# Kernel tuning notes

Measured on AMD Instinct MI355X. Metric: run time of the kernel, lower is better.

## Reference

```python
import jax, jax.numpy as jnp
import numpy as np

K = 2  # diffusion order
N, S, D, L, C = 4000, 32, 128, 2, 10
THETA = 0.5


def setup_inputs() -> dict:
    key = jax.random.key(0)
    ks = jax.random.split(key, 16)
    w = 0.05  # weight scale to keep tanh/exp in sane range
    return {
        "A": jax.random.uniform(ks[0], (N, N), dtype=jnp.float32),
        "embs": jax.random.normal(ks[1], (L, S, N, D), dtype=jnp.float32),
        "conv1_w": jax.random.normal(ks[2], (K, D, D), dtype=jnp.float32) * w,
        "conv2_w": jax.random.normal(ks[3], (K, D, D), dtype=jnp.float32) * w,
        "lin_in_w": jax.random.normal(ks[4], (D, D), dtype=jnp.float32) * w,
        "lin_out_w": jax.random.normal(ks[5], (D, 2 * D), dtype=jnp.float32) * w,
        "W_psi": jax.random.normal(ks[6], (2 * D, D), dtype=jnp.float32) * w,
        "b_psi": jax.random.normal(ks[7], (D,), dtype=jnp.float32) * w,
        "ae": jax.random.uniform(ks[8], (N, 1, 1), dtype=jnp.float32),
        "ab": jax.random.uniform(ks[9], (N, 1, 1), dtype=jnp.float32),
        "emb_table": jax.random.uniform(ks[10], (N, D), minval=-0.1, maxval=0.1, dtype=jnp.float32),
        "W_p": jax.random.normal(ks[11], (D, C), dtype=jnp.float32) * w,
        "W_c": jax.random.normal(ks[12], (D, D), dtype=jnp.float32) * w,
    }


def _diffusion(A_tilde, X, W):
    # A_tilde: [N,N] (sym-normalized); X: [N,S,D] (linear in X, so batching over S
    # is identical to the per-timestep loop); W: [K,D,D]
    P_f = A_tilde / A_tilde.sum(axis=1, keepdims=True)
    P_v = A_tilde.T / A_tilde.sum(axis=0, keepdims=True)
    Z = jnp.einsum('mn,nsd->msd', P_f, X) @ W[0]
    P_psi_f, P_psi_v = P_f, P_v
    for k in range(1, K):
        if k < K // 2:
            P_psi_f = P_psi_f @ P_f
            M = P_psi_f
        else:
            P_psi_v = P_psi_v @ P_v
            M = P_psi_v
        Z = Z + jnp.einsum('mn,nsd->msd', M, X) @ W[k]
    return Z


def _attention(context, lin_in_w, lin_out_w, ae, ab):
    # context: [N,S,D]; query is the last timestep, output_len == 1
    q = context[:, -1, :] @ lin_in_w.T                    # [N,D]
    scores = jnp.einsum('nd,nsd->ns', q, context)         # [N,S]
    attw = jax.nn.softmax(scores, axis=-1)                # [N,S]
    mix = attw[:, None, :] * context.transpose(0, 2, 1)   # [N,D,S]
    delta_t = jnp.arange(S - 1, -1, -1, dtype=context.dtype)  # flipped arange
    bt = jnp.exp(-ab * delta_t[None, None, :])            # [N,1,S]
    term2 = jax.nn.relu(ae * mix * bt)                    # [N,D,S]
    mix_sum = (term2 + mix).sum(axis=-1)                  # [N,D]
    combined = jnp.concatenate([mix_sum, q], axis=-1)     # [N,2D]
    return jnp.tanh(combined @ lin_out_w.T)               # [N,D]


def reference(A, embs, conv1_w, conv2_w, lin_in_w, lin_out_w, W_psi, b_psi,
              ae, ab, emb_table, W_p, W_c):
    n = A.shape[0]
    A_t = A + jnp.eye(n, dtype=A.dtype)
    d_inv_sqrt = A_t.sum(axis=1) ** -0.5
    A_tilde = d_inv_sqrt[:, None] * A_t * d_inv_sqrt[None, :]

    outs = []
    for l in range(L):
        X = embs[l].transpose(1, 0, 2)                    # [N,S,D]
        h = _diffusion(A_tilde, X, conv1_w)
        h = jax.nn.relu(h)
        h = _diffusion(A_tilde, h, conv2_w)               # [N,S,D]
        # fusion with theta = 0.5 (h_tilde is the raw embedding)
        fused = jnp.concatenate([THETA * h, (1.0 - THETA) * X], axis=-1) @ W_psi + b_psi
        outs.append(_attention(fused, lin_in_w, lin_out_w, ae, ab))
    outputs = jnp.stack(outs)                             # [L,N,D]

    # embedding lookup over arange(N) is an identity gather
    qs = jax.nn.relu(emb_table)                           # [N,D]
    betas = jnp.exp(jnp.einsum('nd,lne->lde', qs, jnp.tanh(outputs)))  # [L,D,D]
    betas = betas / betas.sum(axis=0)
    Z = jnp.einsum('lnd,lde->ne', outputs, betas)         # [N,D]

    P = jax.nn.softmax(Z @ W_p, axis=1)                   # [N,C]
    C_mat = P.T @ Z                                       # [C,D]
    eta = P.T @ A @ P                                     # [C,C] (vectorized eta_ij)
    C_prime = jax.nn.relu(eta @ (C_mat @ W_c.T))          # [C,D]
    return P @ C_prime                                    # [N,D]
```

## Files before the change

### kernel.cpp

```cpp
#include <hip/hip_runtime.h>
#include <hip/hip_bf16.h>


typedef __attribute__((ext_vector_type(8))) short short8;
typedef __attribute__((ext_vector_type(4))) float f32x4;
typedef __attribute__((ext_vector_type(4))) unsigned short us4;

__device__ __forceinline__ unsigned short f2bf(float x) {
  unsigned int u = __builtin_bit_cast(unsigned int, x);
  u += 0x7FFFu + ((u >> 16) & 1u);
  return (unsigned short)(u >> 16);
}
__device__ __forceinline__ float bf2f(unsigned short u) {
  unsigned int x = ((unsigned int)u) << 16;
  return __builtin_bit_cast(float, x);
}

__device__ __forceinline__ void gload16(const void* g, void* l) {
  __builtin_amdgcn_global_load_lds((const __attribute__((address_space(1))) void*)g,
                                   (__attribute__((address_space(3))) void*)l, 16, 0, 0);
}

__device__ __forceinline__ void barrier_() {
  __builtin_amdgcn_sched_barrier(0);
  asm volatile("" ::: "memory");
  __builtin_amdgcn_s_barrier();
  asm volatile("" ::: "memory");
  __builtin_amdgcn_sched_barrier(0);
}

template<int TRANS, int RELU>
__global__ __launch_bounds__(512, 2)
void gemm256(const unsigned short* __restrict__ Ap, int lda,
             const unsigned short* __restrict__ Bp, int ldb,
             unsigned short* __restrict__ outp, int ldo, int K)
{
  __shared__ alignas(16) unsigned short lds[81920];
  const int t = threadIdx.x;
  const int lane = t & 63;
  const int wave = t >> 6;
  const int wm = wave >> 2;
  const int wn = wave & 3;
  const int lrow = lane & 15;
  const int kgrp = lane >> 4;
  const int slotbase = (kgrp ^ (lrow & 7)) << 3;

  const int b = blockIdx.x;
  const int wg = (b & 7) * 32 + (b >> 3);
  const int m0 = (wg >> 4) << 8;
  const int j0 = (wg & 15) << 8;

  const int prow = t >> 3;
  const int lslot = (t & 7) ^ (prow & 7);
  const unsigned short* srcA = Ap + (size_t)(m0 + prow) * lda + lslot * 8;
  const unsigned short* srcB = Bp + (size_t)(j0 + prow) * ldb + lslot * 8;
  const size_t a64 = (size_t)64 * lda, a128 = (size_t)128 * lda;
  const size_t b64 = (size_t)64 * ldb, b128 = (size_t)128 * ldb;
  unsigned short* dA = &lds[t * 8];
  unsigned short* dB = &lds[32768 + t * 8];
  const int NT = K >> 6;

#define STG_A(h, kb, kt) { const unsigned short* s_ = srcA + (h)*a128 + (size_t)(kt)*64; \
    gload16(s_, dA + (kb)*16384 + (h)*8192); \
    gload16(s_ + a64, dA + (kb)*16384 + (h)*8192 + 4096); }
#define STG_B(h, bb, kt) { const unsigned short* s_ = srcB + (h)*b128 + (size_t)(kt)*64; \
    gload16(s_, dB + (bb)*16384 + (h)*8192); \
    gload16(s_ + b64, dB + (bb)*16384 + (h)*8192 + 4096); }

  const int arb = wm * 8192 + lrow * 64 + slotbase;
  const int brb = (wn >> 1) * 8192 + ((wn & 1) << 12) + lrow * 64 + slotbase;

#define RD_A(dst, base_off) \
  _Pragma("unroll") for (int mf_ = 0; mf_ < 4; ++mf_) { \
    dst[mf_][0] = *(const short8*)&lds[(base_off) + mf_*1024]; \
    dst[mf_][1] = *(const short8*)&lds[((base_off) ^ 32) + mf_*1024]; }
#define RD_B(dst, base_off) \
  _Pragma("unroll") for (int nf_ = 0; nf_ < 2; ++nf_) { \
    dst[nf_][0] = *(const short8*)&lds[(base_off) + nf_*1024]; \
    dst[nf_][1] = *(const short8*)&lds[((base_off) ^ 32) + nf_*1024]; }

#define MFMA16(AF, BF, MB, NB) \
  _Pragma("unroll") for (int mf_ = 0; mf_ < 4; ++mf_) \
  _Pragma("unroll") for (int nf_ = 0; nf_ < 2; ++nf_) { \
    acc[(MB)+mf_][(NB)+nf_] = __builtin_amdgcn_mfma_f32_16x16x32_bf16(AF[mf_][0], BF[nf_][0], acc[(MB)+mf_][(NB)+nf_], 0,0,0); \
    acc[(MB)+mf_][(NB)+nf_] = __builtin_amdgcn_mfma_f32_16x16x32_bf16(AF[mf_][1], BF[nf_][1], acc[(MB)+mf_][(NB)+nf_], 0,0,0); }

#define LGKM(n) { asm volatile("s_waitcnt lgkmcnt(" #n ")" ::: "memory"); \
                  __builtin_amdgcn_sched_barrier(0); }

  f32x4 acc[8][4];
#pragma unroll
  for (int i = 0; i < 8; ++i)
#pragma unroll
    for (int j = 0; j < 4; ++j) acc[i][j] = f32x4{0.f, 0.f, 0.f, 0.f};

  short8 a0[4][2], a1[4][2], b0[2][2], b1[2][2];

  STG_B(0, 0, 0); STG_B(1, 0, 0); STG_A(0, 0, 0); STG_A(1, 0, 0);
  STG_B(0, 1, 1); STG_B(1, 1, 1); STG_A(0, 1, 1); STG_A(1, 1, 1);
  asm volatile("s_waitcnt vmcnt(8)" ::: "memory");
  barrier_();
  RD_A(a0, arb);
  RD_B(b0, 32768 + brb);

  int rb3 = 0, rn3 = 1, sb3 = 2;
  for (int V = 0; V < NT; ++V) {
    const int abuf  = (V & 1) << 14;
    const int anbuf = ((V + 1) & 1) << 14;
    const int bbuf  = 32768 + (rb3 << 14);
    const int bnbuf = 32768 + (rn3 << 14);
    const bool stg = (V + 2 < NT);
    const bool rdn = (V + 1 < NT);

    RD_B(b1, bbuf + brb + 2048);
    LGKM(4);
    if (stg) STG_B(0, sb3, V + 2);
    __builtin_amdgcn_s_setprio(1);
    MFMA16(a0, b0, 0, 0);
    __builtin_amdgcn_s_setprio(0);
    barrier_();

    RD_A(a1, abuf + arb + 4096);
    LGKM(8);
    if (stg) STG_B(1, sb3, V + 2);
    __builtin_amdgcn_s_setprio(1);
    MFMA16(a0, b1, 0, 2);
    __builtin_amdgcn_s_setprio(0);
    if (stg) { asm volatile("s_waitcnt vmcnt(4)" ::: "memory"); }
    else     { asm volatile("s_waitcnt vmcnt(0)" ::: "memory"); }
    barrier_();

    if (rdn) { RD_A(a0, anbuf + arb); LGKM(8); }
    else     { LGKM(0); }
    if (stg) STG_A(0, (V & 1), V + 2);
    __builtin_amdgcn_s_setprio(1);
    MFMA16(a1, b0, 4, 0);
    __builtin_amdgcn_s_setprio(0);
    barrier_();

    if (rdn) { RD_B(b0, bnbuf + brb); LGKM(4); }
    else     { LGKM(0); }
    if (stg) STG_A(1, (V & 1), V + 2);
    __builtin_amdgcn_s_setprio(1);
    MFMA16(a1, b1, 4, 2);
    __builtin_amdgcn_s_setprio(0);
    barrier_();

    rb3 = rn3; rn3 = (rn3 == 2) ? 0 : rn3 + 1;
    sb3 = (sb3 == 2) ? 0 : sb3 + 1;
  }

#pragma unroll
  for (int mf = 0; mf < 8; ++mf) {
#pragma unroll
    for (int nf = 0; nf < 4; ++nf) {
      const int m = m0 + wm * 128 + mf * 16 + kgrp * 4;
      const int j = j0 + wn * 64 + nf * 16 + lrow;
      if (TRANS) {
        us4 pk;
#pragma unroll
        for (int r = 0; r < 4; ++r) pk[r] = f2bf(acc[mf][nf][r]);
        *(us4*)(outp + (size_t)j * ldo + m) = pk;
      } else {
#pragma unroll
        for (int r = 0; r < 4; ++r) {
          float v = acc[mf][nf][r];
          if (RELU) v = fmaxf(v, 0.f);
          outp[(size_t)(m + r) * ldo + j] = f2bf(v);
        }
      }
    }
  }
#undef STG_A
#undef STG_B
#undef RD_A
#undef RD_B
#undef MFMA16
#undef LGKM
}

template<int EPI, int KFULL, int MINB>
__global__ __launch_bounds__(256, MINB)
void gemm_smallk(const unsigned short* __restrict__ A1,
                 const unsigned short* __restrict__ A2,
                 int k_switch, int a_zstride, int lda,
                 const unsigned short* __restrict__ B, int ldb,
                 void* __restrict__ outp,
                 long o_j, long o_m, long o_z, long o_jt,
                 const float* __restrict__ bias)
{
  __shared__ alignas(16) unsigned short At[(KFULL / 32) * 4096];
  __shared__ alignas(16) unsigned short Bt[(KFULL / 32) * 4096];
  const int t = threadIdx.x;
  const int lane = t & 63;
  const int wave = t >> 6;
  const int m0 = blockIdx.x << 7;
  const int jt = blockIdx.y;
  const int j0 = jt << 7;
  const int z  = blockIdx.z;
  const int wm = (wave >> 1) << 6;
  const int wn = (wave & 1) << 6;
  const int lrow = lane & 15;
  const int kgrp = lane >> 4;

  const unsigned short* A1z = A1 + (long)z * a_zstride;
  const unsigned short* A2z = A2 + (long)z * a_zstride;

  const int r0 = t >> 2, q0 = t & 3;
  const int c1 = t + 256;
  const int r1 = c1 >> 2, q1 = c1 & 3;

#pragma unroll
  for (int kk = 0; kk < KFULL / 32; ++kk) {
    const int k0 = kk * 32;
    const unsigned short* As; int ka;
    if (k0 < k_switch) { As = A1z; ka = k0; } else { As = A2z; ka = k0 - k_switch; }
    gload16(As + (long)(m0 + r0) * lda + ka + q0 * 8, At + kk * 4096 + t * 8);
    gload16(As + (long)(m0 + r1) * lda + ka + q1 * 8, At + kk * 4096 + c1 * 8);
    gload16(B  + (long)(j0 + r0) * ldb + k0 + q0 * 8, Bt + kk * 4096 + t * 8);
    gload16(B  + (long)(j0 + r1) * ldb + k0 + q1 * 8, Bt + kk * 4096 + c1 * 8);
  }
  __syncthreads();

  f32x4 acc[4][4];
#pragma unroll
  for (int i = 0; i < 4; ++i)
#pragma unroll
    for (int j = 0; j < 4; ++j) acc[i][j] = f32x4{0.f, 0.f, 0.f, 0.f};

#pragma unroll
  for (int kk = 0; kk < KFULL / 32; ++kk) {
    short8 af[4], bv[4];
#pragma unroll
    for (int i = 0; i < 4; ++i)
      af[i] = *(const short8*)(At + kk * 4096 + (wm + i * 16 + lrow) * 32 + kgrp * 8);
#pragma unroll
    for (int i = 0; i < 4; ++i)
      bv[i] = *(const short8*)(Bt + kk * 4096 + (wn + i * 16 + lrow) * 32 + kgrp * 8);
#pragma unroll
    for (int i = 0; i < 4; ++i)
#pragma unroll
      for (int j = 0; j < 4; ++j)
        acc[i][j] = __builtin_amdgcn_mfma_f32_16x16x32_bf16(af[i], bv[j], acc[i][j], 0, 0, 0);
  }

  const int mlb = wm + kgrp * 4;
#pragma unroll
  for (int i = 0; i < 4; ++i) {
#pragma unroll
    for (int j = 0; j < 4; ++j) {
      const int jl = wn + j * 16 + lrow;
      const int ml = mlb + i * 16;
      if (EPI == 0) {
        long base = (long)jl * o_j + (long)(m0 + ml) * o_m + (long)z * o_z + (long)jt * o_jt;
        us4 pk;
#pragma unroll
        for (int r = 0; r < 4; ++r) pk[r] = f2bf(acc[i][j][r]);
        *(us4*)((unsigned short*)outp + base) = pk;
      } else if (EPI == 2) {
        float* of = (float*)outp;
        float badd = bias[j0 + jl];
#pragma unroll
        for (int r = 0; r < 4; ++r) {
          long idx = (long)jl * o_j + (long)(m0 + ml + r) * o_m + (long)z * o_z + (long)jt * o_jt;
          of[idx] = acc[i][j][r] + badd;
        }
      } else {
        float* of = (float*)outp;
#pragma unroll
        for (int r = 0; r < 4; ++r) {
          int mm = m0 + ml + r;
          int n = mm & 4095, l = mm >> 12;
          if (n < 4000)
            of[(size_t)l * 512000 + (size_t)n * 128 + (j0 + jl)] = tanhf(acc[i][j][r]);
        }
      }
    }
  }
}

__global__ __launch_bounds__(256) void rowsum_dis(const float* __restrict__ A,
                                                  float* __restrict__ dis) {
  int m = blockIdx.x;
  if (m >= 4000) { if (threadIdx.x == 0) dis[m] = 0.f; return; }
  const float* r = A + (long)m * 4000;
  float a = 0.f;
  for (int i = threadIdx.x; i < 1000; i += 256) {
    float4 v = ((const float4*)r)[i];
    a += v.x + v.y + v.z + v.w;
  }
  for (int o = 32; o; o >>= 1) a += __shfl_xor(a, o);
  __shared__ float ls[4];
  if ((threadIdx.x & 63) == 0) ls[threadIdx.x >> 6] = a;
  __syncthreads();
  if (threadIdx.x == 0) dis[m] = rsqrtf(1.f + ls[0] + ls[1] + ls[2] + ls[3]);
}

__global__ __launch_bounds__(256) void wrow_kernel(const float* __restrict__ A,
                                                   const float* __restrict__ dis,
                                                   float* __restrict__ iwrow) {
  int m = blockIdx.x;
  if (m >= 4000) { if (threadIdx.x == 0) iwrow[m] = 0.f; return; }
  const float* r = A + (long)m * 4000;
  float a = 0.f;
  for (int n = threadIdx.x; n < 4000; n += 256) a += r[n] * dis[n];
  for (int o = 32; o; o >>= 1) a += __shfl_xor(a, o);
  __shared__ float ls[4];
  if ((threadIdx.x & 63) == 0) ls[threadIdx.x >> 6] = a;
  __syncthreads();
  if (threadIdx.x == 0) iwrow[m] = 1.f / (ls[0] + ls[1] + ls[2] + ls[3] + dis[m]);
}

__global__ __launch_bounds__(256) void wcol_part(const float* __restrict__ A,
                                                 const float* __restrict__ dis,
                                                 float* __restrict__ part) {
  int j = blockIdx.x * 256 + threadIdx.x;
  int mz = blockIdx.y;
  float a = 0.f;
  if (j < 4000) {
    int ms = mz * 125;
    for (int m = ms; m < ms + 125; ++m) a += A[(long)m * 4000 + j] * dis[m];
  }
  part[(long)mz * 4096 + j] = a;
}

__global__ __launch_bounds__(256) void wcol_fin(const float* __restrict__ part,
                                                const float* __restrict__ dis,
                                                float* __restrict__ iwcol) {
  int j = blockIdx.x * 256 + threadIdx.x;
  float s = 0.f;
  for (int z = 0; z < 32; ++z) s += part[(long)z * 4096 + j];
  iwcol[j] = (j < 4000) ? 1.f / (s + dis[j]) : 0.f;
}

__global__ __launch_bounds__(256) void build_P(const float* __restrict__ A,
                                               const float* __restrict__ dis,
                                               const float* __restrict__ iwrow,
                                               const float* __restrict__ iwcol,
                                               unsigned short* __restrict__ Pcat,
                                               unsigned short* __restrict__ PV,
                                               unsigned short* __restrict__ PVT) {
  __shared__ float tile[64][65];
  int m0 = blockIdx.y * 64, n0 = blockIdx.x * 64;
#pragma unroll
  for (int i = 0; i < 16; ++i) {
    int idx = i * 256 + threadIdx.x;
    int lr = idx >> 6, lc = idx & 63;
    int m = m0 + lr, n = n0 + lc;
    float v = 0.f;
    if (m < 4000 && n < 4000) {
      float a = A[(long)m * 4000 + n];
      if (m == n) a += 1.f;
      v = a * dis[n];
    }
    Pcat[(long)m * 8192 + n] = f2bf(v * iwrow[m]);
    float pv = v * iwcol[m];
    PVT[(long)m * 4096 + n] = f2bf(pv);
    tile[lr][lc] = pv;
  }
  __syncthreads();
#pragma unroll
  for (int i = 0; i < 16; ++i) {
    int idx = i * 256 + threadIdx.x;
    int lr = idx >> 6, lc = idx & 63;
    PV[(long)(n0 + lr) * 4096 + (m0 + lc)] = f2bf(tile[lc][lr]);
  }
}

__global__ __launch_bounds__(256) void prep_weights(const float* __restrict__ lin_out,
                                                    const float* __restrict__ c1,
                                                    const float* __restrict__ c2,
                                                    const float* __restrict__ wpsi,
                                                    unsigned short* __restrict__ CW1T,
                                                    unsigned short* __restrict__ CW2T,
                                                    unsigned short* __restrict__ WPST,
                                                    unsigned short* __restrict__ LWOB) {
  int i = blockIdx.x * 256 + threadIdx.x;
  if (i < 32768) {
    int j = i >> 7, kk = i & 127;
    CW1T[i] = f2bf(c1[(j >> 7) * 16384 + kk * 128 + (j & 127)]);
  } else if (i < 65536) {
    int k = i - 32768; int j = k >> 7, kk = k & 127;
    CW2T[k] = f2bf(c2[(j >> 7) * 16384 + kk * 128 + (j & 127)]);
  } else if (i < 98304) {
    int k = i - 65536; int e = k >> 8, d2 = k & 255;
    WPST[k] = f2bf(0.5f * wpsi[d2 * 128 + e]);
  } else if (i < 131072) {
    int k = i - 98304;
    LWOB[k] = f2bf(lin_out[k]);
  }
}

__global__ __launch_bounds__(256) void wq_prep(const float* __restrict__ lin_in,
                                               const float* __restrict__ bpsi,
                                               const unsigned short* __restrict__ WPST,
                                               unsigned short* __restrict__ WQ,
                                               float* __restrict__ BQ) {
  int b = blockIdx.x, t = threadIdx.x;
  if (b < 128) {
    int idx = b * 256 + t;
    int d = idx >> 8, k2 = idx & 255;
    float acc = 0.f;
    for (int e = 0; e < 128; ++e)
      acc += lin_in[d * 128 + e] * bf2f(WPST[e * 256 + k2]);
    WQ[idx] = f2bf(acc);
  } else if (t < 128) {
    float acc = 0.f;
    for (int e = 0; e < 128; ++e) acc += bpsi[e] * lin_in[t * 128 + e];
    BQ[t] = acc;
  }
}

__global__ __launch_bounds__(256) void convert_X(const float* __restrict__ embsL,
                                                 unsigned short* __restrict__ X) {
  long i4 = (long)blockIdx.x * 256 + threadIdx.x;
  long e = i4 << 2;
  int n = (int)(e >> 12);
  int r = (int)(e & 4095);
  us4 o;
  if (n < 4000) {
    int s = r >> 7, d = r & 127;
    float4 v = *(const float4*)(embsL + ((long)s * 4000 + n) * 128 + d);
    o[0] = f2bf(v.x); o[1] = f2bf(v.y); o[2] = f2bf(v.z); o[3] = f2bf(v.w);
  } else { o[0] = o[1] = o[2] = o[3] = 0; }
  *(us4*)(X + (long)n * 4096 + r) = o;
}

__global__ __launch_bounds__(128) void attention2(const float* __restrict__ F,
                                                  const float* __restrict__ Q,
                                                  const float* __restrict__ ae,
                                                  const float* __restrict__ ab,
                                                  unsigned short* __restrict__ CATl) {
  int n = blockIdx.x, t = threadIdx.x;
  if (n >= 4000) {
    CATl[(size_t)n * 256 + t] = 0;
    CATl[(size_t)n * 256 + 128 + t] = 0;
    return;
  }
  __shared__ float Fs[32 * 132];
  __shared__ float qv[128], attw[32], btv[32];
  const float* Fr = F + (long)n * 4096;
  for (int i = t; i < 4096; i += 128) { int s = i >> 7, d = i & 127; Fs[s * 132 + d] = Fr[i]; }
  qv[t] = Q[(long)n * 128 + t];
  __syncthreads();
  if (t < 32) {
    float sc = 0.f;
    for (int d = 0; d < 128; ++d) sc += qv[d] * Fs[t * 132 + d];
    float mx = sc;
    for (int o = 16; o; o >>= 1) mx = fmaxf(mx, __shfl_xor(mx, o, 32));
    float ex = expf(sc - mx), sm = ex;
    for (int o = 16; o; o >>= 1) sm += __shfl_xor(sm, o, 32);
    attw[t] = ex / sm;
  } else if (t >= 64 && t < 96) {
    int s = t - 64;
    btv[s] = expf(-ab[n] * (float)(31 - s));
  }
  __syncthreads();
  float aen = ae[n], acc = 0.f;
  for (int s = 0; s < 32; ++s) {
    float f = Fs[s * 132 + t];
    acc += attw[s] * (f + aen * btv[s] * fmaxf(f, 0.f));
  }
  CATl[(size_t)n * 256 + t] = f2bf(acc);
  CATl[(size_t)n * 256 + 128 + t] = f2bf(qv[t]);
}

__global__ __launch_bounds__(256) void tanh_qs(const float* __restrict__ outs,
                                               const float* __restrict__ embt,
                                               float* __restrict__ T, float* __restrict__ qs) {
  long i = (long)blockIdx.x * 256 + threadIdx.x;
  if (i < 1024000) T[i] = tanhf(outs[i]);
  else { long j = i - 1024000; if (j < 512000) qs[j] = fmaxf(embt[j], 0.f); }
}

__global__ __launch_bounds__(256) void betas_part(const float* __restrict__ qs,
                                                  const float* __restrict__ T,
                                                  float* __restrict__ out) {
  int e = threadIdx.x & 127, dl = threadIdx.x >> 7;
  int d = blockIdx.x * 2 + dl, l = blockIdx.y, nc = blockIdx.z;
  const float* Tl = T + (long)l * 512000;
  float acc = 0.f;
  int n0 = nc * 500;
  for (int n = n0; n < n0 + 500; ++n)
    acc += qs[(long)n * 128 + d] * Tl[(long)n * 128 + e];
  out[(long)nc * 32768 + (long)l * 16384 + d * 128 + e] = acc;
}

__global__ __launch_bounds__(256) void bnorm_kernel(const float* __restrict__ brawp,
                                                    float* __restrict__ bn) {
  int i = blockIdx.x * 256 + threadIdx.x;
  float s0 = 0.f, s1 = 0.f;
  for (int nc = 0; nc < 8; ++nc) {
    s0 += brawp[(long)nc * 32768 + i];
    s1 += brawp[(long)nc * 32768 + 16384 + i];
  }
  float b0 = expf(s0), b1 = expf(s1);
  float s = b0 + b1;
  bn[i] = b0 / s;
  bn[16384 + i] = b1 / s;
}

__global__ __launch_bounds__(256) void z_kernel(const float* __restrict__ outs,
                                                const float* __restrict__ bn,
                                                float* __restrict__ Zb) {
  int n = blockIdx.x * 2 + (threadIdx.x >> 7);
  int e = threadIdx.x & 127;
  float acc = 0.f;
  for (int l = 0; l < 2; ++l) {
    const float* orow = outs + ((long)l * 4000 + n) * 128;
    const float* brow = bn + (long)l * 16384;
    for (int d = 0; d < 128; ++d) acc += orow[d] * brow[d * 128 + e];
  }
  Zb[(long)n * 128 + e] = acc;
}

__global__ __launch_bounds__(256) void p_kernel(const float* __restrict__ Zb,
                                                const float* __restrict__ Wp,
                                                float* __restrict__ P) {
  int n = blockIdx.x * 4 + (threadIdx.x >> 6);
  int c = threadIdx.x & 63;
  float val = 0.f;
  if (c < 10) {
    const float* zr = Zb + (long)n * 128;
    for (int d = 0; d < 128; ++d) val += zr[d] * Wp[d * 10 + c];
  }
  float mx = val;
  for (int i = 0; i < 10; ++i) mx = fmaxf(mx, __shfl(val, i, 64));
  float ex = (c < 10) ? expf(val - mx) : 0.f;
  float sm = 0.f;
  for (int i = 0; i < 10; ++i) sm += __shfl(ex, i, 64);
  if (c < 12) P[(long)n * 12 + c] = (c < 10) ? ex / sm : 0.f;
}

__global__ __launch_bounds__(256) void ap_kernel(const float* __restrict__ A,
                                                 const float* __restrict__ P,
                                                 float* __restrict__ AP) {
  int m = blockIdx.x, t = threadIdx.x;
  const float* Ar = A + (long)m * 4000;
  float acc[10];
#pragma unroll
  for (int c = 0; c < 10; ++c) acc[c] = 0.f;
  for (int n = t; n < 4000; n += 256) {
    float a = Ar[n];
    const float* Pr = P + (long)n * 12;
#pragma unroll
    for (int c = 0; c < 10; ++c) acc[c] += a * Pr[c];
  }
#pragma unroll
  for (int c = 0; c < 10; ++c)
    for (int o = 32; o; o >>= 1) acc[c] += __shfl_xor(acc[c], o);
  __shared__ float ls[4][10];
  if ((t & 63) == 0)
    for (int c = 0; c < 10; ++c) ls[t >> 6][c] = acc[c];
  __syncthreads();
  if (t < 10) AP[(long)m * 12 + t] = ls[0][t] + ls[1][t] + ls[2][t] + ls[3][t];
  if (t >= 10 && t < 12) AP[(long)m * 12 + t] = 0.f;
}

__global__ __launch_bounds__(256) void etacm_part(const float* __restrict__ P,
                                                  const float* __restrict__ AP,
                                                  const float* __restrict__ Z,
                                                  float* __restrict__ peta,
                                                  float* __restrict__ pcm) {
  int b = blockIdx.x, t = threadIdx.x;
  int ms = b * 63, me = ms + 63; if (me > 4000) me = 4000;
  int i_ = t / 10, j_ = t % 10;
  float ea = 0.f;
  float ca[5];
#pragma unroll
  for (int k = 0; k < 5; ++k) ca[k] = 0.f;
  for (int m = ms; m < me; ++m) {
    if (t < 100) ea += P[(long)m * 12 + i_] * AP[(long)m * 12 + j_];
#pragma unroll
    for (int k = 0; k < 5; ++k) {
      int idx = t + 256 * k;
      int c = idx >> 7, e = idx & 127;
      ca[k] += P[(long)m * 12 + c] * Z[(long)m * 128 + e];
    }
  }
  if (t < 100) peta[(long)b * 100 + t] = ea;
#pragma unroll
  for (int k = 0; k < 5; ++k) pcm[(long)b * 1280 + t + 256 * k] = ca[k];
}

__global__ __launch_bounds__(256) void final_small(const float* __restrict__ peta,
                                                   const float* __restrict__ pcm,
                                                   const float* __restrict__ Wc,
                                                   float* __restrict__ cprime) {
  __shared__ float eta_s[100], cm_s[1280], tmp_s[1280];
  int t = threadIdx.x;
  if (t < 100) {
    float s = 0.f;
    for (int b = 0; b < 64; ++b) s += peta[(long)b * 100 + t];
    eta_s[t] = s;
  }
  for (int i = t; i < 1280; i += 256) {
    float s = 0.f;
    for (int b = 0; b < 64; ++b) s += pcm[(long)b * 1280 + i];
    cm_s[i] = s;
  }
  __syncthreads();
  for (int i = t; i < 1280; i += 256) {
    int c = i >> 7, d = i & 127;
    float s = 0.f;
    for (int e = 0; e < 128; ++e) s += cm_s[c * 128 + e] * Wc[d * 128 + e];
    tmp_s[i] = s;
  }
  __syncthreads();
  for (int i = t; i < 1280; i += 256) {
    int c = i >> 7, d = i & 127;
    float s = 0.f;
    for (int j = 0; j < 10; ++j) s += eta_s[c * 10 + j] * tmp_s[j * 128 + d];
    cprime[i] = fmaxf(s, 0.f);
  }
}

__global__ __launch_bounds__(256) void out_kernel(const float* __restrict__ P,
                                                  const float* __restrict__ cpr,
                                                  float* __restrict__ out) {
  int idx = blockIdx.x * 256 + threadIdx.x;
  int n = idx >> 7, d = idx & 127;
  float s = 0.f;
#pragma unroll
  for (int c = 0; c < 10; ++c) s += P[(long)n * 12 + c] * cpr[c * 128 + d];
  out[idx] = s;
}

extern "C" void kernel_launch(void* const* d_in, const int* in_sizes, int n_in,
                              void* d_out, int out_size, void* d_ws, size_t ws_size,
                              hipStream_t stream) {
  (void)in_sizes; (void)n_in; (void)out_size; (void)ws_size;
  const float* A      = (const float*)d_in[0];
  const float* embs   = (const float*)d_in[1];
  const float* conv1w = (const float*)d_in[2];
  const float* conv2w = (const float*)d_in[3];
  const float* lin_in = (const float*)d_in[4];
  const float* lin_out= (const float*)d_in[5];
  const float* Wpsi   = (const float*)d_in[6];
  const float* bpsi   = (const float*)d_in[7];
  const float* ae     = (const float*)d_in[8];
  const float* ab     = (const float*)d_in[9];
  const float* embt   = (const float*)d_in[10];
  const float* Wp     = (const float*)d_in[11];
  const float* Wc     = (const float*)d_in[12];
  float* out = (float*)d_out;
  char* ws = (char*)d_ws;

  size_t off = 0;
  auto alloc = [&](size_t b) { size_t r = off; off += (b + 255) & ~(size_t)255; return r; };
  unsigned short* PCAT = (unsigned short*)(ws + alloc((size_t)4096 * 8192 * 2));
  char*           BTF  = ws + alloc((size_t)4096 * 8192 * 2);
  unsigned short* BT   = (unsigned short*)BTF;
  float*          Ff   = (float*)BTF;
  unsigned short* XBF  = (unsigned short*)(ws + alloc((size_t)4096 * 4096 * 2));
  unsigned short* PV   = XBF;
  unsigned short* HBUF = (unsigned short*)(ws + alloc((size_t)4096 * 4096 * 2));
  unsigned short* PVT  = HBUF;
  float* DIS   = (float*)(ws + alloc(4096 * 4));
  float* IWROW = (float*)(ws + alloc(4096 * 4));
  float* IWCOL = (float*)(ws + alloc(4096 * 4));
  float* WCP   = (float*)(ws + alloc((size_t)32 * 4096 * 4));
  unsigned short* CW1T = (unsigned short*)(ws + alloc(32768 * 2));
  unsigned short* CW2T = (unsigned short*)(ws + alloc(32768 * 2));
  unsigned short* WPST = (unsigned short*)(ws + alloc(32768 * 2));
  unsigned short* LWOB = (unsigned short*)(ws + alloc(32768 * 2));
  unsigned short* WQ   = (unsigned short*)(ws + alloc(32768 * 2));
  float* BQ    = (float*)(ws + alloc(128 * 4));
  float* QBUF  = (float*)(ws + alloc((size_t)4096 * 128 * 4));
  unsigned short* CAT = (unsigned short*)(ws + alloc((size_t)8192 * 256 * 2));
  float* OUTS = (float*)(ws + alloc((size_t)2 * 4000 * 128 * 4));
  float* TT   = (float*)(ws + alloc((size_t)2 * 4000 * 128 * 4));
  float* QS   = (float*)(ws + alloc((size_t)4000 * 128 * 4));
  float* BRAWP= (float*)(ws + alloc((size_t)8 * 32768 * 4));
  float* BNRM = (float*)(ws + alloc(32768 * 4));
  float* ZB   = (float*)(ws + alloc((size_t)4000 * 128 * 4));
  float* PP   = (float*)(ws + alloc((size_t)4000 * 12 * 4));
  float* APB  = (float*)(ws + alloc((size_t)4000 * 12 * 4));
  float* PETA = (float*)(ws + alloc((size_t)64 * 100 * 4));
  float* PCM  = (float*)(ws + alloc((size_t)64 * 1280 * 4));
  float* CPR  = (float*)(ws + alloc(1280 * 4));

  const int BIG = 1 << 30;

  rowsum_dis<<<4096, 256, 0, stream>>>(A, DIS);
  wrow_kernel<<<4096, 256, 0, stream>>>(A, DIS, IWROW);
  wcol_part<<<dim3(16, 32), 256, 0, stream>>>(A, DIS, WCP);
  wcol_fin<<<16, 256, 0, stream>>>(WCP, DIS, IWCOL);
  prep_weights<<<512, 256, 0, stream>>>(lin_out, conv1w, conv2w, Wpsi,
                                        CW1T, CW2T, WPST, LWOB);
  wq_prep<<<129, 256, 0, stream>>>(lin_in, bpsi, WPST, WQ, BQ);
  build_P<<<dim3(64, 64), 256, 0, stream>>>(A, DIS, IWROW, IWCOL, PCAT, PV, PVT);

  gemm256<1, 0><<<256, 512, 0, stream>>>(PVT, 4096, PV, 4096, PCAT + 4096, 8192, 4096);

  for (int l = 0; l < 2; ++l) {
    convert_X<<<16384, 256, 0, stream>>>(embs + (long)l * 32 * 4000 * 128, XBF);
    gemm_smallk<0, 128, 2><<<dim3(32, 2, 32), 256, 0, stream>>>(
        XBF, XBF, BIG, 128, 4096, CW1T, 128,
        BT, 8192L, 1L, 128L * 8192, 4096L, nullptr);
    gemm256<0, 1><<<256, 512, 0, stream>>>(PCAT, 8192, BT, 8192, HBUF, 4096, 8192);
    gemm_smallk<0, 128, 2><<<dim3(32, 2, 32), 256, 0, stream>>>(
        HBUF, HBUF, BIG, 128, 4096, CW2T, 128,
        BT, 8192L, 1L, 128L * 8192, 4096L, nullptr);
    gemm256<0, 0><<<256, 512, 0, stream>>>(PCAT, 8192, BT, 8192, HBUF, 4096, 8192);
    gemm_smallk<2, 256, 1><<<dim3(32, 1, 32), 256, 0, stream>>>(
        HBUF, XBF, 128, 128, 4096, WPST, 256,
        Ff, 1L, 4096L, 128L, 0L, bpsi);
    gemm_smallk<2, 256, 1><<<dim3(32, 1, 1), 256, 0, stream>>>(
        HBUF + 31 * 128, XBF + 31 * 128, 128, 0, 4096, WQ, 256,
        QBUF, 1L, 128L, 0L, 0L, BQ);
    attention2<<<4096, 128, 0, stream>>>(Ff, QBUF, ae, ab, CAT + (size_t)l * 4096 * 256);
  }

  gemm_smallk<3, 256, 1><<<dim3(64, 1, 1), 256, 0, stream>>>(
      CAT, CAT, BIG, 0, 256, LWOB, 256,
      OUTS, 0L, 0L, 0L, 0L, nullptr);

  tanh_qs<<<6000, 256, 0, stream>>>(OUTS, embt, TT, QS);
  betas_part<<<dim3(64, 2, 8), 256, 0, stream>>>(QS, TT, BRAWP);
  bnorm_kernel<<<64, 256, 0, stream>>>(BRAWP, BNRM);
  z_kernel<<<2000, 256, 0, stream>>>(OUTS, BNRM, ZB);
  p_kernel<<<1000, 256, 0, stream>>>(ZB, Wp, PP);
  ap_kernel<<<4000, 256, 0, stream>>>(A, PP, APB);
  etacm_part<<<64, 256, 0, stream>>>(PP, APB, ZB, PETA, PCM);
  final_small<<<1, 256, 0, stream>>>(PETA, PCM, Wc, CPR);
  out_kernel<<<2000, 256, 0, stream>>>(PP, CPR, out);
}
```

Measured before the change: 1.544 ms.

## Switch gemm256 B operand from triple to double LDS buffering with reordered staging

Restructures the main bf16 GEMM's software pipeline so that B, like A, uses two LDS buffers instead of three, shrinking the shared-memory footprint from 160KB to 128KB. Global-to-LDS stages and register reads are regrouped across the four MFMA phases, with a barrier and a full lgkmcnt(0) wait before every phase in place of the earlier partial waits. The aim is a simpler schedule and lower LDS use. In exchange, prefetch depth and overlap shrink, and the extra barriers and full waits can stall the MFMA stream.

```diff
diff --git a/kernel.cpp b/kernel.cpp
--- a/kernel.cpp
+++ b/kernel.cpp
@@ -35,7 +35,7 @@
              const unsigned short* __restrict__ Bp, int ldb,
              unsigned short* __restrict__ outp, int ldo, int K)
 {
-  __shared__ alignas(16) unsigned short lds[81920];
+  __shared__ alignas(16) unsigned short lds[65536];
   const int t = threadIdx.x;
   const int lane = t & 63;
   const int wave = t >> 6;
@@ -63,12 +63,12 @@
 #define STG_A(h, kb, kt) { const unsigned short* s_ = srcA + (h)*a128 + (size_t)(kt)*64; \
     gload16(s_, dA + (kb)*16384 + (h)*8192); \
     gload16(s_ + a64, dA + (kb)*16384 + (h)*8192 + 4096); }
-#define STG_B(h, bb, kt) { const unsigned short* s_ = srcB + (h)*b128 + (size_t)(kt)*64; \
-    gload16(s_, dB + (bb)*16384 + (h)*8192); \
-    gload16(s_ + b64, dB + (bb)*16384 + (h)*8192 + 4096); }
+#define STG_B(h, kb, kt) { const unsigned short* s_ = srcB + (h)*b128 + (size_t)(kt)*64; \
+    gload16(s_, dB + (kb)*16384 + (h)*8192); \
+    gload16(s_ + b64, dB + (kb)*16384 + (h)*8192 + 4096); }
 
   const int arb = wm * 8192 + lrow * 64 + slotbase;
-  const int brb = (wn >> 1) * 8192 + ((wn & 1) << 12) + lrow * 64 + slotbase;
+  const int brb = wn * 4096 + lrow * 64 + slotbase;
 
 #define RD_A(dst, base_off) \
   _Pragma("unroll") for (int mf_ = 0; mf_ < 4; ++mf_) { \
@@ -85,8 +85,8 @@
     acc[(MB)+mf_][(NB)+nf_] = __builtin_amdgcn_mfma_f32_16x16x32_bf16(AF[mf_][0], BF[nf_][0], acc[(MB)+mf_][(NB)+nf_], 0,0,0); \
     acc[(MB)+mf_][(NB)+nf_] = __builtin_amdgcn_mfma_f32_16x16x32_bf16(AF[mf_][1], BF[nf_][1], acc[(MB)+mf_][(NB)+nf_], 0,0,0); }
 
-#define LGKM(n) { asm volatile("s_waitcnt lgkmcnt(" #n ")" ::: "memory"); \
-                  __builtin_amdgcn_sched_barrier(0); }
+#define LGKM0 { asm volatile("s_waitcnt lgkmcnt(0)" ::: "memory"); \
+                __builtin_amdgcn_sched_barrier(0); }
 
   f32x4 acc[8][4];
 #pragma unroll
@@ -96,58 +96,50 @@
 
   short8 a0[4][2], a1[4][2], b0[2][2], b1[2][2];
 
-  STG_B(0, 0, 0); STG_B(1, 0, 0); STG_A(0, 0, 0); STG_A(1, 0, 0);
-  STG_B(0, 1, 1); STG_B(1, 1, 1); STG_A(0, 1, 1); STG_A(1, 1, 1);
-  asm volatile("s_waitcnt vmcnt(8)" ::: "memory");
+  STG_A(0, 0, 0); STG_A(1, 0, 0); STG_B(0, 0, 0); STG_B(1, 0, 0);
+  STG_B(0, 1, 1); STG_B(1, 1, 1); STG_A(0, 1, 1);
+  asm volatile("s_waitcnt vmcnt(6)" ::: "memory");
   barrier_();
-  RD_A(a0, arb);
   RD_B(b0, 32768 + brb);
 
-  int rb3 = 0, rn3 = 1, sb3 = 2;
   for (int V = 0; V < NT; ++V) {
-    const int abuf  = (V & 1) << 14;
-    const int anbuf = ((V + 1) & 1) << 14;
-    const int bbuf  = 32768 + (rb3 << 14);
-    const int bnbuf = 32768 + (rn3 << 14);
-    const bool stg = (V + 2 < NT);
-    const bool rdn = (V + 1 < NT);
-
-    RD_B(b1, bbuf + brb + 2048);
-    LGKM(4);
-    if (stg) STG_B(0, sb3, V + 2);
+    const int abuf = (V & 1) << 14;
+    const int bbuf = 32768 + ((V & 1) << 14);
+    const bool st1 = (V + 1 < NT);
+    const bool st2 = (V + 2 < NT);
+
+    RD_A(a0, abuf + arb);
+    if (st1) STG_A(1, (V + 1) & 1, V + 1);
+    barrier_(); LGKM0;
     __builtin_amdgcn_s_setprio(1);
     MFMA16(a0, b0, 0, 0);
     __builtin_amdgcn_s_setprio(0);
     barrier_();
 
-    RD_A(a1, abuf + arb + 4096);
-    LGKM(8);
-    if (stg) STG_B(1, sb3, V + 2);
+    RD_B(b1, bbuf + brb + 2048);
+    barrier_(); LGKM0;
     __builtin_amdgcn_s_setprio(1);
     MFMA16(a0, b1, 0, 2);
     __builtin_amdgcn_s_setprio(0);
-    if (stg) { asm volatile("s_waitcnt vmcnt(4)" ::: "memory"); }
-    else     { asm volatile("s_waitcnt vmcnt(0)" ::: "memory"); }
     barrier_();
 
-    if (rdn) { RD_A(a0, anbuf + arb); LGKM(8); }
-    else     { LGKM(0); }
-    if (stg) STG_A(0, (V & 1), V + 2);
+    RD_A(a1, abuf + arb + 4096);
+    if (st2) { STG_B(0, V & 1, V + 2); STG_B(1, V & 1, V + 2); }
+    barrier_(); LGKM0;
     __builtin_amdgcn_s_setprio(1);
     MFMA16(a1, b0, 4, 0);
     __builtin_amdgcn_s_setprio(0);
     barrier_();
 
-    if (rdn) { RD_B(b0, bnbuf + brb); LGKM(4); }
-    else     { LGKM(0); }
-    if (stg) STG_A(1, (V & 1), V + 2);
+    if (st2) STG_A(0, V & 1, V + 2);
+    if (st2)      { asm volatile("s_waitcnt vmcnt(6)" ::: "memory"); }
+    else if (st1) { asm volatile("s_waitcnt vmcnt(0)" ::: "memory"); }
+    if (st1) RD_B(b0, 32768 + (((V + 1) & 1) << 14) + brb);
+    barrier_(); LGKM0;
     __builtin_amdgcn_s_setprio(1);
     MFMA16(a1, b1, 4, 2);
     __builtin_amdgcn_s_setprio(0);
     barrier_();
-
-    rb3 = rn3; rn3 = (rn3 == 2) ? 0 : rn3 + 1;
-    sb3 = (sb3 == 2) ? 0 : sb3 + 1;
   }
 
 #pragma unroll
@@ -176,7 +168,7 @@
 #undef RD_A
 #undef RD_B
 #undef MFMA16
-#undef LGKM
+#undef LGKM0
 }
 
 template<int EPI, int KFULL, int MINB>
```

Measured after the change: 1.594 ms. 3.2% more time.

## Stage GEMM epilogues through LDS and fuse query GEMM and tanh pass

Applied to the files above, without the earlier changes.

The transposed epilogue of the large GEMM and the bf16 epilogue of the small-K GEMM now go through a swizzled LDS tile, so global stores are contiguous rows instead of scattered 8-byte writes. The separate query-projection GEMM launch is folded into the fused-projection GEMM as an extra z slice that uses a second weight, output and bias. The tanh_qs kernel is removed: the second tanh is computed in the output-GEMM epilogue, and relu of the embedding table moves into prep_weights. This cuts launches and strided memory traffic at the cost of extra LDS barriers and more epilogue work.

```diff
diff --git a/kernel.cpp b/kernel.cpp
--- a/kernel.cpp
+++ b/kernel.cpp
@@ -150,18 +150,35 @@
     sb3 = (sb3 == 2) ? 0 : sb3 + 1;
   }
 
-#pragma unroll
-  for (int mf = 0; mf < 8; ++mf) {
-#pragma unroll
-    for (int nf = 0; nf < 4; ++nf) {
-      const int m = m0 + wm * 128 + mf * 16 + kgrp * 4;
-      const int j = j0 + wn * 64 + nf * 16 + lrow;
-      if (TRANS) {
+  if (TRANS) {
+#pragma unroll
+    for (int mf = 0; mf < 8; ++mf) {
+#pragma unroll
+      for (int nf = 0; nf < 4; ++nf) {
+        const int ml = wm * 128 + mf * 16 + kgrp * 4;
+        const int jl = wn * 64 + nf * 16 + lrow;
+        const int gm = ml >> 2;
         us4 pk;
 #pragma unroll
         for (int r = 0; r < 4; ++r) pk[r] = f2bf(acc[mf][nf][r]);
-        *(us4*)(outp + (size_t)j * ldo + m) = pk;
-      } else {
+        *(us4*)&lds[jl * 256 + ((gm ^ (jl & 7)) << 2)] = pk;
+      }
+    }
+    barrier_();
+#pragma unroll
+    for (int i = 0; i < 32; ++i) {
+      const int r = i * 8 + (t >> 6);
+      const int c = t & 63;
+      us4 v = *(const us4*)&lds[r * 256 + ((c ^ (r & 7)) << 2)];
+      *(us4*)(outp + (size_t)(j0 + r) * ldo + m0 + c * 4) = v;
+    }
+  } else {
+#pragma unroll
+    for (int mf = 0; mf < 8; ++mf) {
+#pragma unroll
+      for (int nf = 0; nf < 4; ++nf) {
+        const int m = m0 + wm * 128 + mf * 16 + kgrp * 4;
+        const int j = j0 + wn * 64 + nf * 16 + lrow;
 #pragma unroll
         for (int r = 0; r < 4; ++r) {
           float v = acc[mf][nf][r];
@@ -179,7 +196,7 @@
 #undef LGKM
 }
 
-template<int EPI, int KFULL, int MINB>
+template<int EPI, int KFULL, int MINB, int Z32>
 __global__ __launch_bounds__(256, MINB)
 void gemm_smallk(const unsigned short* __restrict__ A1,
                  const unsigned short* __restrict__ A2,
@@ -187,7 +204,10 @@
                  const unsigned short* __restrict__ B, int ldb,
                  void* __restrict__ outp,
                  long o_j, long o_m, long o_z, long o_jt,
-                 const float* __restrict__ bias)
+                 const float* __restrict__ bias,
+                 const unsigned short* __restrict__ B2,
+                 float* __restrict__ out2,
+                 const float* __restrict__ bias2)
 {
   __shared__ alignas(16) unsigned short At[(KFULL / 32) * 4096];
   __shared__ alignas(16) unsigned short Bt[(KFULL / 32) * 4096];
@@ -198,13 +218,16 @@
   const int jt = blockIdx.y;
   const int j0 = jt << 7;
   const int z  = blockIdx.z;
+  const bool isq = Z32 && (z == 32);
+  const int ze = isq ? 31 : z;
+  const unsigned short* Bp = isq ? B2 : B;
   const int wm = (wave >> 1) << 6;
   const int wn = (wave & 1) << 6;
   const int lrow = lane & 15;
   const int kgrp = lane >> 4;
 
-  const unsigned short* A1z = A1 + (long)z * a_zstride;
-  const unsigned short* A2z = A2 + (long)z * a_zstride;
+  const unsigned short* A1z = A1 + (long)ze * a_zstride;
+  const unsigned short* A2z = A2 + (long)ze * a_zstride;
 
   const int r0 = t >> 2, q0 = t & 3;
   const int c1 = t + 256;
@@ -217,8 +240,8 @@
     if (k0 < k_switch) { As = A1z; ka = k0; } else { As = A2z; ka = k0 - k_switch; }
     gload16(As + (long)(m0 + r0) * lda + ka + q0 * 8, At + kk * 4096 + t * 8);
     gload16(As + (long)(m0 + r1) * lda + ka + q1 * 8, At + kk * 4096 + c1 * 8);
-    gload16(B  + (long)(j0 + r0) * ldb + k0 + q0 * 8, Bt + kk * 4096 + t * 8);
-    gload16(B  + (long)(j0 + r1) * ldb + k0 + q1 * 8, Bt + kk * 4096 + c1 * 8);
+    gload16(Bp + (long)(j0 + r0) * ldb + k0 + q0 * 8, Bt + kk * 4096 + t * 8);
+    gload16(Bp + (long)(j0 + r1) * ldb + k0 + q1 * 8, Bt + kk * 4096 + c1 * 8);
   }
   __syncthreads();
 
@@ -245,25 +268,53 @@
   }
 
   const int mlb = wm + kgrp * 4;
+  if (EPI == 0) {
+    __syncthreads();
+#pragma unroll
+    for (int i = 0; i < 4; ++i) {
+#pragma unroll
+      for (int j = 0; j < 4; ++j) {
+        const int jl = wn + j * 16 + lrow;
+        const int ml = mlb + i * 16;
+        const int gm = ml >> 2;
+        us4 pk;
+#pragma unroll
+        for (int r = 0; r < 4; ++r) pk[r] = f2bf(acc[i][j][r]);
+        *(us4*)&At[jl * 128 + ((gm ^ (jl & 7)) << 2)] = pk;
+      }
+    }
+    __syncthreads();
+#pragma unroll
+    for (int i = 0; i < 16; ++i) {
+      const int r = i * 8 + (t >> 5);
+      const int c = t & 31;
+      us4 v = *(const us4*)&At[r * 128 + ((c ^ (r & 7)) << 2)];
+      long base = (long)r * o_j + (long)(m0 + c * 4) * o_m + (long)z * o_z + (long)jt * o_jt;
+      *(us4*)((unsigned short*)outp + base) = v;
+    }
+    return;
+  }
+
 #pragma unroll
   for (int i = 0; i < 4; ++i) {
 #pragma unroll
     for (int j = 0; j < 4; ++j) {
       const int jl = wn + j * 16 + lrow;
       const int ml = mlb + i * 16;
-      if (EPI == 0) {
-        long base = (long)jl * o_j + (long)(m0 + ml) * o_m + (long)z * o_z + (long)jt * o_jt;
-        us4 pk;
-#pragma unroll
-        for (int r = 0; r < 4; ++r) pk[r] = f2bf(acc[i][j][r]);
-        *(us4*)((unsigned short*)outp + base) = pk;
-      } else if (EPI == 2) {
-        float* of = (float*)outp;
-        float badd = bias[j0 + jl];
-#pragma unroll
-        for (int r = 0; r < 4; ++r) {
-          long idx = (long)jl * o_j + (long)(m0 + ml + r) * o_m + (long)z * o_z + (long)jt * o_jt;
-          of[idx] = acc[i][j][r] + badd;
+      if (EPI == 2) {
+        if (isq) {
+          float badd = bias2[j0 + jl];
+#pragma unroll
+          for (int r = 0; r < 4; ++r)
+            out2[(size_t)(m0 + ml + r) * 128 + (j0 + jl)] = acc[i][j][r] + badd;
+        } else {
+          float* of = (float*)outp;
+          float badd = bias[j0 + jl];
+#pragma unroll
+          for (int r = 0; r < 4; ++r) {
+            long idx = (long)jl * o_j + (long)(m0 + ml + r) * o_m + (long)z * o_z + (long)jt * o_jt;
+            of[idx] = acc[i][j][r] + badd;
+          }
         }
       } else {
         float* of = (float*)outp;
@@ -271,8 +322,12 @@
         for (int r = 0; r < 4; ++r) {
           int mm = m0 + ml + r;
           int n = mm & 4095, l = mm >> 12;
-          if (n < 4000)
-            of[(size_t)l * 512000 + (size_t)n * 128 + (j0 + jl)] = tanhf(acc[i][j][r]);
+          if (n < 4000) {
+            float o = tanhf(acc[i][j][r]);
+            size_t idx = (size_t)l * 512000 + (size_t)n * 128 + (j0 + jl);
+            of[idx] = o;
+            out2[idx] = tanhf(o);
+          }
         }
       }
     }
@@ -371,10 +426,12 @@
                                                     const float* __restrict__ c1,
                                                     const float* __restrict__ c2,
                                                     const float* __restrict__ wpsi,
+                                                    const float* __restrict__ embt,
                                                     unsigned short* __restrict__ CW1T,
                                                     unsigned short* __restrict__ CW2T,
                                                     unsigned short* __restrict__ WPST,
-                                                    unsigned short* __restrict__ LWOB) {
+                                                    unsigned short* __restrict__ LWOB,
+                                                    float* __restrict__ qs) {
   int i = blockIdx.x * 256 + threadIdx.x;
   if (i < 32768) {
     int j = i >> 7, kk = i & 127;
@@ -388,6 +445,9 @@
   } else if (i < 131072) {
     int k = i - 98304;
     LWOB[k] = f2bf(lin_out[k]);
+  } else if (i < 643072) {
+    int k = i - 131072;
+    qs[k] = fmaxf(embt[k], 0.f);
   }
 }
 
@@ -463,14 +523,6 @@
   }
   CATl[(size_t)n * 256 + t] = f2bf(acc);
   CATl[(size_t)n * 256 + 128 + t] = f2bf(qv[t]);
-}
-
-__global__ __launch_bounds__(256) void tanh_qs(const float* __restrict__ outs,
-                                               const float* __restrict__ embt,
-                                               float* __restrict__ T, float* __restrict__ qs) {
-  long i = (long)blockIdx.x * 256 + threadIdx.x;
-  if (i < 1024000) T[i] = tanhf(outs[i]);
-  else { long j = i - 1024000; if (j < 512000) qs[j] = fmaxf(embt[j], 0.f); }
 }
 
 __global__ __launch_bounds__(256) void betas_part(const float* __restrict__ qs,
@@ -686,8 +738,8 @@
   wrow_kernel<<<4096, 256, 0, stream>>>(A, DIS, IWROW);
   wcol_part<<<dim3(16, 32), 256, 0, stream>>>(A, DIS, WCP);
   wcol_fin<<<16, 256, 0, stream>>>(WCP, DIS, IWCOL);
-  prep_weights<<<512, 256, 0, stream>>>(lin_out, conv1w, conv2w, Wpsi,
-                                        CW1T, CW2T, WPST, LWOB);
+  prep_weights<<<2512, 256, 0, stream>>>(lin_out, conv1w, conv2w, Wpsi, embt,
+                                         CW1T, CW2T, WPST, LWOB, QS);
   wq_prep<<<129, 256, 0, stream>>>(lin_in, bpsi, WPST, WQ, BQ);
   build_P<<<dim3(64, 64), 256, 0, stream>>>(A, DIS, IWROW, IWCOL, PCAT, PV, PVT);
 
@@ -695,28 +747,24 @@
 
   for (int l = 0; l < 2; ++l) {
     convert_X<<<16384, 256, 0, stream>>>(embs + (long)l * 32 * 4000 * 128, XBF);
-    gemm_smallk<0, 128, 2><<<dim3(32, 2, 32), 256, 0, stream>>>(
+    gemm_smallk<0, 128, 2, 0><<<dim3(32, 2, 32), 256, 0, stream>>>(
         XBF, XBF, BIG, 128, 4096, CW1T, 128,
-        BT, 8192L, 1L, 128L * 8192, 4096L, nullptr);
+        BT, 8192L, 1L, 128L * 8192, 4096L, nullptr, nullptr, nullptr, nullptr);
     gemm256<0, 1><<<256, 512, 0, stream>>>(PCAT, 8192, BT, 8192, HBUF, 4096, 8192);
-    gemm_smallk<0, 128, 2><<<dim3(32, 2, 32), 256, 0, stream>>>(
+    gemm_smallk<0, 128, 2, 0><<<dim3(32, 2, 32), 256, 0, stream>>>(
         HBUF, HBUF, BIG, 128, 4096, CW2T, 128,
-        BT, 8192L, 1L, 128L * 8192, 4096L, nullptr);
+        BT, 8192L, 1L, 128L * 8192, 4096L, nullptr, nullptr, nullptr, nullptr);
     gemm256<0, 0><<<256, 512, 0, stream>>>(PCAT, 8192, BT, 8192, HBUF, 4096, 8192);
-    gemm_smallk<2, 256, 1><<<dim3(32, 1, 32), 256, 0, stream>>>(
+    gemm_smallk<2, 256, 1, 1><<<dim3(32, 1, 33), 256, 0, stream>>>(
         HBUF, XBF, 128, 128, 4096, WPST, 256,
-        Ff, 1L, 4096L, 128L, 0L, bpsi);
-    gemm_smallk<2, 256, 1><<<dim3(32, 1, 1), 256, 0, stream>>>(
-        HBUF + 31 * 128, XBF + 31 * 128, 128, 0, 4096, WQ, 256,
-        QBUF, 1L, 128L, 0L, 0L, BQ);
+        Ff, 1L, 4096L, 128L, 0L, bpsi, WQ, QBUF, BQ);
     attention2<<<4096, 128, 0, stream>>>(Ff, QBUF, ae, ab, CAT + (size_t)l * 4096 * 256);
   }
 
-  gemm_smallk<3, 256, 1><<<dim3(64, 1, 1), 256, 0, stream>>>(
+  gemm_smallk<3, 256, 1, 0><<<dim3(64, 1, 1), 256, 0, stream>>>(
       CAT, CAT, BIG, 0, 256, LWOB, 256,
-      OUTS, 0L, 0L, 0L, 0L, nullptr);
-
-  tanh_qs<<<6000, 256, 0, stream>>>(OUTS, embt, TT, QS);
+      OUTS, 0L, 0L, 0L, 0L, nullptr, nullptr, TT, nullptr);
+
   betas_part<<<dim3(64, 2, 8), 256, 0, stream>>>(QS, TT, BRAWP);
   bnorm_kernel<<<64, 256, 0, stream>>>(BRAWP, BNRM);
   z_kernel<<<2000, 256, 0, stream>>>(OUTS, BNRM, ZB);
```

Result: faster. 1.469 ms (-4.9%).
